# Performance work log

Hardware: AMD Instinct MI355X
Metric: run time of the kernel (lower is better)

Reference implementation:

```python
import jax, jax.numpy as jnp
import numpy as np
from jax import lax

N_SAMPLES = 2 ** 15   # 32768
N_ATOMS = 2048
ATOM_SIZE = 1024
K_SPARSE = 64
BATCH = 4


def setup_inputs() -> dict:
    key = jax.random.key(0)
    k1, k2 = jax.random.split(key)
    orig = jax.random.normal(k1, (BATCH, 1, N_SAMPLES), dtype=jnp.float32)
    # atoms ~ uniform(-1, 1) as in the torch Parameter init
    atoms = jax.random.uniform(k2, (N_ATOMS, ATOM_SIZE), dtype=jnp.float32,
                               minval=-1.0, maxval=1.0)
    return {"orig": orig, "atoms": atoms}


def reference(orig, atoms):
    B = orig.shape[0]
    # Correlate input with the atom dictionary (F.conv1d, padding=atom_size//2).
    x = lax.conv_general_dilated(
        orig, atoms.reshape(N_ATOMS, 1, ATOM_SIZE),
        window_strides=(1,), padding=[(ATOM_SIZE // 2, ATOM_SIZE // 2)],
        dimension_numbers=("NCH", "OIH", "NCH"))  # [B, n_atoms, N+1]
    x = x[..., :N_SAMPLES]                          # [B, n_atoms, N]
    # dropout(p=0.05) omitted (eval-mode / deterministic reference)

    # sparsify: per-batch top-k over the flattened (atom, time) grid
    flat = x.reshape(B, N_ATOMS * N_SAMPLES)
    values, indices = lax.top_k(flat, K_SPARSE)      # [B, K]
    atom_idx = indices // N_SAMPLES                  # [B, K]
    time_idx = indices % N_SAMPLES                   # [B, K]

    # Overlap-add synthesis: gather atom, scale, scatter-add into 2N buffer.
    contrib = atoms[atom_idx] * values[..., None]    # [B, K, atom_size]
    pos = time_idx[..., None] + jnp.arange(ATOM_SIZE)  # [B, K, atom_size]
    b_idx = jnp.arange(B)[:, None, None]
    out = jnp.zeros((B, 2 * N_SAMPLES), dtype=orig.dtype)
    out = out.at[b_idx, pos].add(contrib)
    return out[:, None, :N_SAMPLES]                  # [B, 1, N]
```

## Files before the change

### kernel.cpp

```cpp
#include <hip/hip_runtime.h>

#define NS     32768
#define NA     2048
#define ASZ    1024
#define NB     4
#define SIGC   34848
#define BM     128
#define BN     256
#define TILES  2048
#define CAP    8192
#define MINT   5080
#define SSCALE 20.0f
#define BSTR   1408
#define BSZ    22528

typedef signed char s8;
typedef __attribute__((ext_vector_type(4))) int i32x4;

__device__ __forceinline__ int imax(int a, int b) { return a > b ? a : b; }

__global__ void prep_k(const float* __restrict__ atoms, const float* __restrict__ orig,
                       s8* __restrict__ apack, s8* __restrict__ sigsh,
                       float* __restrict__ sigf, int* __restrict__ wlc) {
  if (blockIdx.x == 0 && threadIdx.x == 0) *wlc = 0;
  if (blockIdx.x < 1024) {
    int g = blockIdx.x >> 3, kt = blockIdx.x & 7;
    int t = threadIdx.x;
    int kk = t >> 7, r = t & 127, l = r >> 1, half = r & 1;
    int row = g * 16 + (l & 15);
    int kbase = kt * 128 + (kk * 4 + (l >> 4)) * 16 + half * 8;
    const float* srow = atoms + (size_t)row * ASZ + kbase;
    s8* dst = apack + (size_t)(((g * 8 + kt) * 2 + kk) << 10) + l * 16 + half * 8;
    #pragma unroll
    for (int j = 0; j < 8; j++) {
      float q = fminf(127.f, fmaxf(-127.f, srow[j] * 127.f));
      dst[j] = (s8)__float2int_rn(q);
    }
  } else {
    int r = blockIdx.x - 1024;
    int nch = (SIGC + 255) / 256;
    int bm = r / nch, chunk = r % nch;
    int i = chunk * 256 + threadIdx.x;
    if (i >= SIGC) return;
    int b = bm >> 4, m = bm & 15;
    int j = i + m - 512;
    float f = (j >= 0 && j < NS) ? orig[(size_t)b * NS + j] : 0.0f;
    float q = fminf(127.f, fmaxf(-127.f, f * SSCALE));
    sigsh[(size_t)bm * SIGC + i] = (s8)__float2int_rn(q);
    if (m == 0) sigf[(size_t)b * SIGC + i] = f;
  }
}

__device__ __forceinline__ void stage_bsig(const s8* __restrict__ Sb, int t0,
                                           s8* Bsig, int w, int lane) {
  #pragma unroll
  for (int i = 0; i < 3; i++) {
    int c = w + 8 * i;
    if (c < 22) {
      int o = c * 1024 + lane * 16;
      int m = o / BSTR;
      int pp = (o - m * BSTR) >> 4;
      int s = (pp & ~7) | ((pp ^ m) & 7);
      const s8* src = Sb + (size_t)m * SIGC + t0 + (s << 4);
      __builtin_amdgcn_global_load_lds((const __attribute__((address_space(1))) void*)src,
          (__attribute__((address_space(3))) void*)(&Bsig[c * 1024]), 16, 0, 0);
    }
  }
}

__device__ __forceinline__ void compute_tile(const s8* __restrict__ Apk, const s8* Bsig, int kt,
                                             int w, int lane, i32x4 acc[4][4]) {
  int wr = w >> 2, wc = w & 3;
  int kgrp = lane >> 4;
  int m = lane & 15, mx = m & 7;
  const s8* brow = Bsig + m * BSTR;
  const s8* abase = Apk + ((((size_t)wr * 4 * 8 + kt) * 2) << 10) + (lane << 4);
  int sb = wc * 4 + kgrp + kt * 8;
  #pragma unroll
  for (int kk = 0; kk < 2; kk++) {
    i32x4 af[4], bfr[4];
    #pragma unroll
    for (int mf = 0; mf < 4; mf++)
      af[mf] = *(const i32x4*)&abase[((mf * 16 + kk) << 10)];
    #pragma unroll
    for (int nf = 0; nf < 4; nf++) {
      int s = sb + nf + kk * 4;
      int ps = (s & ~7) | ((s ^ mx) & 7);
      bfr[nf] = *(const i32x4*)&brow[ps << 4];
    }
    __builtin_amdgcn_s_setprio(1);
    #pragma unroll
    for (int mf = 0; mf < 4; mf++)
      #pragma unroll
      for (int nf = 0; nf < 4; nf++)
        acc[mf][nf] = __builtin_amdgcn_mfma_i32_16x16x64_i8(af[mf], bfr[nf], acc[mf][nf], 0, 0, 0);
    __builtin_amdgcn_s_setprio(0);
  }
}

__global__ __launch_bounds__(512, 4)
void screen1(const s8* __restrict__ apack, const s8* __restrict__ sigsh,
             int* __restrict__ tmax)
{
  __shared__ __align__(16) s8 Bsig[BSZ];
  __shared__ int wred[8];
  int bid0 = blockIdx.x;
  int bid  = (bid0 & 7) * ((NB * TILES) >> 3) + (bid0 >> 3);
  int b = bid >> 11, tile = bid & (TILES - 1);
  int mt = tile >> 7, nt = tile & 127;
  int m0 = mt * BM, t0 = nt * BN;
  int tid = threadIdx.x, w = tid >> 6, lane = tid & 63;
  const s8* Apk = apack + (size_t)mt * 131072;
  const s8* Sb = sigsh + (size_t)b * 16 * SIGC;

  i32x4 acc[4][4];
  #pragma unroll
  for (int i = 0; i < 4; i++)
    #pragma unroll
    for (int j = 0; j < 4; j++) acc[i][j] = (i32x4){0, 0, 0, 0};

  stage_bsig(Sb, t0, Bsig, w, lane);
  __syncthreads();
  #pragma unroll 2
  for (int kt = 0; kt < 8; kt++)
    compute_tile(Apk, Bsig, kt, w, lane, acc);

  int lmax = -2147483647;
  #pragma unroll
  for (int mf = 0; mf < 4; mf++)
    #pragma unroll
    for (int nf = 0; nf < 4; nf++)
      #pragma unroll
      for (int q = 0; q < 4; q++) lmax = imax(lmax, acc[mf][nf][q]);
  #pragma unroll
  for (int off = 32; off; off >>= 1) lmax = imax(lmax, __shfl_xor(lmax, off, 64));
  if (lane == 0) wred[w] = lmax;
  __syncthreads();
  if (tid == 0) {
    int mm = wred[0];
    #pragma unroll
    for (int i = 1; i < 8; i++) mm = imax(mm, wred[i]);
    tmax[b * TILES + tile] = mm;
  }
}

__global__ void thresh_k(const int* __restrict__ tmax, int* __restrict__ thr,
                         int* __restrict__ ccnt, int* __restrict__ wl, int* __restrict__ wlc) {
  int b = blockIdx.x, tid = threadIdx.x;
  __shared__ int hist[4096];
  __shared__ int tsum[256];
  __shared__ int hist2[256];
  __shared__ int sB1, sAbove, sThr;
  for (int i = tid; i < 4096; i += 256) hist[i] = 0;
  __syncthreads();
  for (int i = tid; i < TILES; i += 256) {
    unsigned u = (unsigned)tmax[b * TILES + i] ^ 0x80000000u;
    atomicAdd(&hist[u >> 20], 1);
  }
  __syncthreads();
  { int s = 0;
    for (int j = 0; j < 16; j++) s += hist[tid * 16 + j];
    tsum[tid] = s; }
  __syncthreads();
  if (tid == 0) {
    int cum = 0, T = 0;
    for (int t2 = 255; t2 >= 0; t2--) {
      if (cum + tsum[t2] >= 64) { T = t2; break; }
      cum += tsum[t2];
    }
    int B1 = T * 16;
    for (int bk = T * 16 + 15; bk >= T * 16; bk--) {
      if (cum + hist[bk] >= 64) { B1 = bk; break; }
      cum += hist[bk];
    }
    sB1 = B1; sAbove = cum;
  }
  __syncthreads();
  if (tid < 256) hist2[tid] = 0;
  __syncthreads();
  int B1 = sB1;
  for (int i = tid; i < TILES; i += 256) {
    unsigned u = (unsigned)tmax[b * TILES + i] ^ 0x80000000u;
    if ((int)(u >> 20) == B1) atomicAdd(&hist2[(u >> 12) & 255], 1);
  }
  __syncthreads();
  if (tid == 0) {
    int cum = sAbove, B2 = 0;
    for (int z = 255; z >= 0; z--) { cum += hist2[z]; if (cum >= 64) { B2 = z; break; } }
    unsigned ulow = ((unsigned)B1 << 20) | ((unsigned)B2 << 12);
    int t = (int)(ulow ^ 0x80000000u);
    sThr = t; thr[b] = t; ccnt[b] = 0;
  }
  __syncthreads();
  int cut = sThr - MINT;
  for (int i = tid; i < TILES; i += 256)
    if (tmax[b * TILES + i] >= cut) { int p = atomicAdd(wlc, 1); wl[p] = (b << 11) | i; }
}

__global__ __launch_bounds__(512, 4)
void screen2(const s8* __restrict__ apack, const s8* __restrict__ sigsh,
             const int* __restrict__ thr, const int* __restrict__ wl,
             const int* __restrict__ wlc, int* __restrict__ ccnt, int* __restrict__ cidx)
{
  __shared__ __align__(16) s8 Bsig[BSZ];
  int n = *wlc; if (n > NB * TILES) n = NB * TILES;
  int tid = threadIdx.x, w = tid >> 6, lane = tid & 63;
  int wr = w >> 2, wc = w & 3;
  int kgrp = lane >> 4;

  for (int wi = blockIdx.x; wi < n; wi += gridDim.x) {
    int e = wl[wi];
    int b = e >> 11, tile = e & (TILES - 1);
    int cut = thr[b] - MINT;
    int mt = tile >> 7, nt = tile & 127;
    int m0 = mt * BM, t0 = nt * BN;
    const s8* Apk = apack + (size_t)mt * 131072;
    const s8* Sb = sigsh + (size_t)b * 16 * SIGC;

    i32x4 acc[4][4];
    #pragma unroll
    for (int i = 0; i < 4; i++)
      #pragma unroll
      for (int j = 0; j < 4; j++) acc[i][j] = (i32x4){0, 0, 0, 0};

    stage_bsig(Sb, t0, Bsig, w, lane);
    __syncthreads();
    #pragma unroll 2
    for (int kt = 0; kt < 8; kt++)
      compute_tile(Apk, Bsig, kt, w, lane, acc);

    int rb = m0 + wr * 64 + 4 * kgrp;
    int cb = t0 + wc * 64 + (lane & 15);
    #pragma unroll
    for (int mf = 0; mf < 4; mf++)
      #pragma unroll
      for (int nf = 0; nf < 4; nf++)
        #pragma unroll
        for (int q = 0; q < 4; q++) {
          if (acc[mf][nf][q] >= cut) {
            int a = rb + mf * 16 + q;
            int t = cb + nf * 16;
            int p = atomicAdd(&ccnt[b], 1);
            if (p < CAP) cidx[b * CAP + p] = (a << 15) | t;
          }
        }
    __syncthreads();
  }
}

__global__ void rescore_k(const float* __restrict__ atoms, const float* __restrict__ sigf,
                          const int* __restrict__ ccnt, const int* __restrict__ cidx,
                          float* __restrict__ cval) {
  int nwv = gridDim.x * 4;
  int gw = blockIdx.x * 4 + (threadIdx.x >> 6);
  int lane = threadIdx.x & 63;
  for (int b = 0; b < NB; b++) {
    int cnt = ccnt[b]; if (cnt > CAP) cnt = CAP;
    for (int ci = gw; ci < cnt; ci += nwv) {
      int idx = cidx[b * CAP + ci];
      int a = idx >> 15, t = idx & (NS - 1);
      const float* ap = atoms + (size_t)a * ASZ;
      const float* sp = sigf + (size_t)b * SIGC + t;
      float sum = 0.f;
      #pragma unroll
      for (int j = 0; j < 16; j++) { int k = lane + 64 * j; sum += ap[k] * sp[k]; }
      #pragma unroll
      for (int off = 32; off; off >>= 1) sum += __shfl_xor(sum, off, 64);
      if (lane == 0) cval[b * CAP + ci] = sum;
    }
  }
}

__global__ void select_k(const int* __restrict__ ccnt, const float* __restrict__ cval,
                         const int* __restrict__ cidx, float* __restrict__ sval,
                         int* __restrict__ sidx) {
  int b = blockIdx.x, tid = threadIdx.x;
  int cnt = ccnt[b]; if (cnt > CAP) cnt = CAP;
  __shared__ float lv[2048];
  __shared__ int li[2048];
  for (int ii = 0; ii * 256 < cnt; ii++) {
    int i = ii * 256 + tid;
    float vi = 0.f; int idi = 0; bool act = i < cnt;
    if (act) { vi = cval[b * CAP + i]; idi = cidx[b * CAP + i]; }
    int rank = 0;
    for (int c0 = 0; c0 < cnt; c0 += 2048) {
      int mchunk = cnt - c0; if (mchunk > 2048) mchunk = 2048;
      __syncthreads();
      for (int j = tid; j < mchunk; j += 256) {
        lv[j] = cval[b * CAP + c0 + j];
        li[j] = cidx[b * CAP + c0 + j];
      }
      __syncthreads();
      if (act)
        for (int j = 0; j < mchunk; j++)
          rank += (lv[j] > vi) || (lv[j] == vi && li[j] < idi);
    }
    if (act && rank < 64) { sval[b * 64 + rank] = vi; sidx[b * 64 + rank] = idi; }
  }
}

__global__ void recon_k(const float* __restrict__ atoms, const float* __restrict__ sval,
                        const int* __restrict__ sidx, float* __restrict__ out) {
  int gp = blockIdx.x * 256 + threadIdx.x;
  int b = gp >> 15, p = gp & (NS - 1);
  __shared__ float vv[64];
  __shared__ int ii[64];
  if (threadIdx.x < 64) {
    vv[threadIdx.x] = sval[b * 64 + threadIdx.x];
    ii[threadIdx.x] = sidx[b * 64 + threadIdx.x];
  }
  __syncthreads();
  float acc = 0.f;
  for (int s = 0; s < 64; s++) {
    int idx = ii[s];
    int a = idx >> 15, t = idx & (NS - 1);
    int off = p - t;
    if (off >= 0 && off < ASZ) acc += vv[s] * atoms[(size_t)a * ASZ + off];
  }
  out[gp] = acc;
}

extern "C" void kernel_launch(void* const* d_in, const int* in_sizes, int n_in,
                              void* d_out, int out_size, void* d_ws, size_t ws_size,
                              hipStream_t stream) {
  const float* orig  = (const float*)d_in[0];
  const float* atoms = (const float*)d_in[1];
  float* out = (float*)d_out;
  char* ws = (char*)d_ws;

  s8*    apack = (s8*)   (ws + 0);
  s8*    sigsh = (s8*)   (ws + 2097152);
  float* sigf  = (float*)(ws + 4327424);
  int*   tmax  = (int*)  (ws + 4884992);
  int*   thr   = (int*)  (ws + 4917760);
  int*   ccnt  = (int*)  (ws + 4918016);
  float* cval  = (float*)(ws + 4918272);
  int*   cidx  = (int*)  (ws + 5049344);
  float* sval  = (float*)(ws + 5180416);
  int*   sidx  = (int*)  (ws + 5181440);
  int*   wl    = (int*)  (ws + 5182464);
  int*   wlc   = (int*)  (ws + 5215232);

  int nch = (SIGC + 255) / 256;
  prep_k<<<1024 + NB * 16 * nch, 256, 0, stream>>>(atoms, orig, apack, sigsh, sigf, wlc);
  screen1<<<NB * TILES, 512, 0, stream>>>(apack, sigsh, tmax);
  thresh_k<<<NB, 256, 0, stream>>>(tmax, thr, ccnt, wl, wlc);
  screen2<<<256, 512, 0, stream>>>(apack, sigsh, thr, wl, wlc, ccnt, cidx);
  rescore_k<<<128, 256, 0, stream>>>(atoms, sigf, ccnt, cidx, cval);
  select_k<<<NB, 256, 0, stream>>>(ccnt, cval, cidx, sval, sidx);
  recon_k<<<out_size / 256, 256, 0, stream>>>(atoms, sval, sidx, out);
}
```

Measured before the change: 269.7 us.

## Widen screening tiles and make screen1 persistent with double-buffered signal staging

Doubles the time-tile width to 512 samples and uses 1024-thread workgroups with 16 waves, so each A-fragment load feeds twice as many columns. screen1 becomes a persistent kernel of 256 workgroups that prefetches the next tile's shifted signal into a second LDS buffer while computing the current one. This aims to cut A-matrix reload traffic and hide LDS staging latency. In exchange it uses more LDS per block, lowers occupancy, adds an extra barrier per tile, and screen2 now processes coarser worklist tiles, which may include more wasted work past the threshold.

Measured after the change: 281.8 us. +4.5%, slower.

```diff
diff --git a/kernel.cpp b/kernel.cpp
--- a/kernel.cpp
+++ b/kernel.cpp
@@ -6,13 +6,14 @@
 #define NB     4
 #define SIGC   34848
 #define BM     128
-#define BN     256
-#define TILES  2048
+#define BN     512
+#define TILES  1024
+#define NWG    4096
 #define CAP    8192
 #define MINT   5080
 #define SSCALE 20.0f
-#define BSTR   1408
-#define BSZ    22528
+#define BSTR   1664
+#define BSZ    26624
 
 typedef signed char s8;
 typedef __attribute__((ext_vector_type(4))) int i32x4;
@@ -54,9 +55,9 @@
 __device__ __forceinline__ void stage_bsig(const s8* __restrict__ Sb, int t0,
                                            s8* Bsig, int w, int lane) {
   #pragma unroll
-  for (int i = 0; i < 3; i++) {
-    int c = w + 8 * i;
-    if (c < 22) {
+  for (int i = 0; i < 2; i++) {
+    int c = w + 16 * i;
+    if (c < 26) {
       int o = c * 1024 + lane * 16;
       int m = o / BSTR;
       int pp = (o - m * BSTR) >> 4;
@@ -70,7 +71,7 @@
 
 __device__ __forceinline__ void compute_tile(const s8* __restrict__ Apk, const s8* Bsig, int kt,
                                              int w, int lane, i32x4 acc[4][4]) {
-  int wr = w >> 2, wc = w & 3;
+  int wr = w >> 3, wc = w & 7;
   int kgrp = lane >> 4;
   int m = lane & 15, mx = m & 7;
   const s8* brow = Bsig + m * BSTR;
@@ -98,49 +99,60 @@
   }
 }
 
-__global__ __launch_bounds__(512, 4)
+#define DECODE(x, b_, mt_, nt_) { int bb = ((x) & 7) * (NWG >> 3) + ((x) >> 3); \
+  b_ = bb >> 10; int tl = bb & (TILES - 1); mt_ = tl >> 6; nt_ = tl & 63; }
+
+__global__ __launch_bounds__(1024, 4)
 void screen1(const s8* __restrict__ apack, const s8* __restrict__ sigsh,
              int* __restrict__ tmax)
 {
-  __shared__ __align__(16) s8 Bsig[BSZ];
-  __shared__ int wred[8];
-  int bid0 = blockIdx.x;
-  int bid  = (bid0 & 7) * ((NB * TILES) >> 3) + (bid0 >> 3);
-  int b = bid >> 11, tile = bid & (TILES - 1);
-  int mt = tile >> 7, nt = tile & 127;
-  int m0 = mt * BM, t0 = nt * BN;
+  __shared__ __align__(16) s8 Bsig[2][BSZ];
+  __shared__ int wred[16];
   int tid = threadIdx.x, w = tid >> 6, lane = tid & 63;
-  const s8* Apk = apack + (size_t)mt * 131072;
-  const s8* Sb = sigsh + (size_t)b * 16 * SIGC;
-
-  i32x4 acc[4][4];
-  #pragma unroll
-  for (int i = 0; i < 4; i++)
-    #pragma unroll
-    for (int j = 0; j < 4; j++) acc[i][j] = (i32x4){0, 0, 0, 0};
-
-  stage_bsig(Sb, t0, Bsig, w, lane);
-  __syncthreads();
-  #pragma unroll 2
-  for (int kt = 0; kt < 8; kt++)
-    compute_tile(Apk, Bsig, kt, w, lane, acc);
-
-  int lmax = -2147483647;
-  #pragma unroll
-  for (int mf = 0; mf < 4; mf++)
-    #pragma unroll
-    for (int nf = 0; nf < 4; nf++)
-      #pragma unroll
-      for (int q = 0; q < 4; q++) lmax = imax(lmax, acc[mf][nf][q]);
-  #pragma unroll
-  for (int off = 32; off; off >>= 1) lmax = imax(lmax, __shfl_xor(lmax, off, 64));
-  if (lane == 0) wred[w] = lmax;
-  __syncthreads();
-  if (tid == 0) {
-    int mm = wred[0];
-    #pragma unroll
-    for (int i = 1; i < 8; i++) mm = imax(mm, wred[i]);
-    tmax[b * TILES + tile] = mm;
+
+  int b, mt, nt;
+  DECODE(blockIdx.x, b, mt, nt);
+  stage_bsig(sigsh + (size_t)b * 16 * SIGC, nt * BN, Bsig[0], w, lane);
+  __syncthreads();
+  int cur = 0;
+
+  for (int x = blockIdx.x; x < NWG; x += 256) {
+    int xn = x + 256;
+    int bn = 0, mtn = 0, ntn = 0;
+    if (xn < NWG) {
+      DECODE(xn, bn, mtn, ntn);
+      stage_bsig(sigsh + (size_t)bn * 16 * SIGC, ntn * BN, Bsig[cur ^ 1], w, lane);
+    }
+
+    const s8* Apk = apack + (size_t)mt * 131072;
+    i32x4 acc[4][4];
+    #pragma unroll
+    for (int i = 0; i < 4; i++)
+      #pragma unroll
+      for (int j = 0; j < 4; j++) acc[i][j] = (i32x4){0, 0, 0, 0};
+    #pragma unroll 2
+    for (int kt = 0; kt < 8; kt++)
+      compute_tile(Apk, Bsig[cur], kt, w, lane, acc);
+
+    int lmax = -2147483647;
+    #pragma unroll
+    for (int mf = 0; mf < 4; mf++)
+      #pragma unroll
+      for (int nf = 0; nf < 4; nf++)
+        #pragma unroll
+        for (int q = 0; q < 4; q++) lmax = imax(lmax, acc[mf][nf][q]);
+    #pragma unroll
+    for (int off = 32; off; off >>= 1) lmax = imax(lmax, __shfl_xor(lmax, off, 64));
+    if (lane == 0) wred[w] = lmax;
+    __syncthreads();
+    if (tid == 0) {
+      int mm = wred[0];
+      #pragma unroll
+      for (int i = 1; i < 16; i++) mm = imax(mm, wred[i]);
+      tmax[b * TILES + (mt << 6 | nt)] = mm;
+    }
+    __syncthreads();
+    cur ^= 1; b = bn; mt = mtn; nt = ntn;
   }
 }
 
@@ -194,25 +206,25 @@
   __syncthreads();
   int cut = sThr - MINT;
   for (int i = tid; i < TILES; i += 256)
-    if (tmax[b * TILES + i] >= cut) { int p = atomicAdd(wlc, 1); wl[p] = (b << 11) | i; }
-}
-
-__global__ __launch_bounds__(512, 4)
+    if (tmax[b * TILES + i] >= cut) { int p = atomicAdd(wlc, 1); wl[p] = (b << 10) | i; }
+}
+
+__global__ __launch_bounds__(1024, 4)
 void screen2(const s8* __restrict__ apack, const s8* __restrict__ sigsh,
              const int* __restrict__ thr, const int* __restrict__ wl,
              const int* __restrict__ wlc, int* __restrict__ ccnt, int* __restrict__ cidx)
 {
   __shared__ __align__(16) s8 Bsig[BSZ];
-  int n = *wlc; if (n > NB * TILES) n = NB * TILES;
+  int n = *wlc; if (n > NWG) n = NWG;
   int tid = threadIdx.x, w = tid >> 6, lane = tid & 63;
-  int wr = w >> 2, wc = w & 3;
+  int wr = w >> 3, wc = w & 7;
   int kgrp = lane >> 4;
 
   for (int wi = blockIdx.x; wi < n; wi += gridDim.x) {
     int e = wl[wi];
-    int b = e >> 11, tile = e & (TILES - 1);
+    int b = e >> 10, tile = e & (TILES - 1);
     int cut = thr[b] - MINT;
-    int mt = tile >> 7, nt = tile & 127;
+    int mt = tile >> 6, nt = tile & 63;
     int m0 = mt * BM, t0 = nt * BN;
     const s8* Apk = apack + (size_t)mt * 131072;
     const s8* Sb = sigsh + (size_t)b * 16 * SIGC;
@@ -332,20 +344,20 @@
   s8*    sigsh = (s8*)   (ws + 2097152);
   float* sigf  = (float*)(ws + 4327424);
   int*   tmax  = (int*)  (ws + 4884992);
-  int*   thr   = (int*)  (ws + 4917760);
-  int*   ccnt  = (int*)  (ws + 4918016);
-  float* cval  = (float*)(ws + 4918272);
-  int*   cidx  = (int*)  (ws + 5049344);
-  float* sval  = (float*)(ws + 5180416);
-  int*   sidx  = (int*)  (ws + 5181440);
-  int*   wl    = (int*)  (ws + 5182464);
-  int*   wlc   = (int*)  (ws + 5215232);
+  int*   thr   = (int*)  (ws + 4901376);
+  int*   ccnt  = (int*)  (ws + 4901632);
+  float* cval  = (float*)(ws + 4901888);
+  int*   cidx  = (int*)  (ws + 5032960);
+  float* sval  = (float*)(ws + 5164032);
+  int*   sidx  = (int*)  (ws + 5165056);
+  int*   wl    = (int*)  (ws + 5166080);
+  int*   wlc   = (int*)  (ws + 5182464);
 
   int nch = (SIGC + 255) / 256;
   prep_k<<<1024 + NB * 16 * nch, 256, 0, stream>>>(atoms, orig, apack, sigsh, sigf, wlc);
-  screen1<<<NB * TILES, 512, 0, stream>>>(apack, sigsh, tmax);
+  screen1<<<256, 1024, 0, stream>>>(apack, sigsh, tmax);
   thresh_k<<<NB, 256, 0, stream>>>(tmax, thr, ccnt, wl, wlc);
-  screen2<<<256, 512, 0, stream>>>(apack, sigsh, thr, wl, wlc, ccnt, cidx);
+  screen2<<<256, 1024, 0, stream>>>(apack, sigsh, thr, wl, wlc, ccnt, cidx);
   rescore_k<<<128, 256, 0, stream>>>(atoms, sigf, ccnt, cidx, cval);
   select_k<<<NB, 256, 0, stream>>>(ccnt, cval, cidx, sval, sidx);
   recon_k<<<out_size / 256, 256, 0, stream>>>(atoms, sval, sidx, out);
```

## Make screen1 persistent with double-buffered signal staging across tiles

Applied to the files above, without the earlier changes.

Screen1 moves from one workgroup per tile (8192 blocks) to 512 persistent workgroups that loop over tiles. The next tile's signal window is staged into a second LDS buffer while the current tile's MFMA work runs, to overlap global loads with compute and cut launch and prologue cost. The cost is that LDS use doubles (about 45 KB per block), which may lower occupancy. An extra barrier per iteration and a fixed grid that may not evenly fill the CUs add further risk.

Result: slower. 278.7 us (+3.3%).

```diff
diff --git a/kernel.cpp b/kernel.cpp
--- a/kernel.cpp
+++ b/kernel.cpp
@@ -8,6 +8,7 @@
 #define BM     128
 #define BN     256
 #define TILES  2048
+#define NWG    8192
 #define CAP    8192
 #define MINT   5080
 #define SSCALE 20.0f
@@ -98,49 +99,60 @@
   }
 }
 
+#define DECODE(x, b_, mt_, nt_) { int bb = ((x) & 7) * (NWG >> 3) + ((x) >> 3); \
+  b_ = bb >> 11; int tl = bb & (TILES - 1); mt_ = tl >> 7; nt_ = tl & 127; }
+
 __global__ __launch_bounds__(512, 4)
 void screen1(const s8* __restrict__ apack, const s8* __restrict__ sigsh,
              int* __restrict__ tmax)
 {
-  __shared__ __align__(16) s8 Bsig[BSZ];
+  __shared__ __align__(16) s8 Bsig[2][BSZ];
   __shared__ int wred[8];
-  int bid0 = blockIdx.x;
-  int bid  = (bid0 & 7) * ((NB * TILES) >> 3) + (bid0 >> 3);
-  int b = bid >> 11, tile = bid & (TILES - 1);
-  int mt = tile >> 7, nt = tile & 127;
-  int m0 = mt * BM, t0 = nt * BN;
   int tid = threadIdx.x, w = tid >> 6, lane = tid & 63;
-  const s8* Apk = apack + (size_t)mt * 131072;
-  const s8* Sb = sigsh + (size_t)b * 16 * SIGC;
-
-  i32x4 acc[4][4];
-  #pragma unroll
-  for (int i = 0; i < 4; i++)
-    #pragma unroll
-    for (int j = 0; j < 4; j++) acc[i][j] = (i32x4){0, 0, 0, 0};
-
-  stage_bsig(Sb, t0, Bsig, w, lane);
-  __syncthreads();
-  #pragma unroll 2
-  for (int kt = 0; kt < 8; kt++)
-    compute_tile(Apk, Bsig, kt, w, lane, acc);
-
-  int lmax = -2147483647;
-  #pragma unroll
-  for (int mf = 0; mf < 4; mf++)
-    #pragma unroll
-    for (int nf = 0; nf < 4; nf++)
-      #pragma unroll
-      for (int q = 0; q < 4; q++) lmax = imax(lmax, acc[mf][nf][q]);
-  #pragma unroll
-  for (int off = 32; off; off >>= 1) lmax = imax(lmax, __shfl_xor(lmax, off, 64));
-  if (lane == 0) wred[w] = lmax;
-  __syncthreads();
-  if (tid == 0) {
-    int mm = wred[0];
-    #pragma unroll
-    for (int i = 1; i < 8; i++) mm = imax(mm, wred[i]);
-    tmax[b * TILES + tile] = mm;
+
+  int b, mt, nt;
+  DECODE(blockIdx.x, b, mt, nt);
+  stage_bsig(sigsh + (size_t)b * 16 * SIGC, nt * BN, Bsig[0], w, lane);
+  __syncthreads();
+  int cur = 0;
+
+  for (int x = blockIdx.x; x < NWG; x += 512) {
+    int xn = x + 512;
+    int bn = 0, mtn = 0, ntn = 0;
+    if (xn < NWG) {
+      DECODE(xn, bn, mtn, ntn);
+      stage_bsig(sigsh + (size_t)bn * 16 * SIGC, ntn * BN, Bsig[cur ^ 1], w, lane);
+    }
+
+    const s8* Apk = apack + (size_t)mt * 131072;
+    i32x4 acc[4][4];
+    #pragma unroll
+    for (int i = 0; i < 4; i++)
+      #pragma unroll
+      for (int j = 0; j < 4; j++) acc[i][j] = (i32x4){0, 0, 0, 0};
+    #pragma unroll 2
+    for (int kt = 0; kt < 8; kt++)
+      compute_tile(Apk, Bsig[cur], kt, w, lane, acc);
+
+    int lmax = -2147483647;
+    #pragma unroll
+    for (int mf = 0; mf < 4; mf++)
+      #pragma unroll
+      for (int nf = 0; nf < 4; nf++)
+        #pragma unroll
+        for (int q = 0; q < 4; q++) lmax = imax(lmax, acc[mf][nf][q]);
+    #pragma unroll
+    for (int off = 32; off; off >>= 1) lmax = imax(lmax, __shfl_xor(lmax, off, 64));
+    if (lane == 0) wred[w] = lmax;
+    __syncthreads();
+    if (tid == 0) {
+      int mm = wred[0];
+      #pragma unroll
+      for (int i = 1; i < 8; i++) mm = imax(mm, wred[i]);
+      tmax[b * TILES + (mt << 7 | nt)] = mm;
+    }
+    __syncthreads();
+    cur ^= 1; b = bn; mt = mtn; nt = ntn;
   }
 }
 
@@ -203,7 +215,7 @@
              const int* __restrict__ wlc, int* __restrict__ ccnt, int* __restrict__ cidx)
 {
   __shared__ __align__(16) s8 Bsig[BSZ];
-  int n = *wlc; if (n > NB * TILES) n = NB * TILES;
+  int n = *wlc; if (n > NWG) n = NWG;
   int tid = threadIdx.x, w = tid >> 6, lane = tid & 63;
   int wr = w >> 2, wc = w & 3;
   int kgrp = lane >> 4;
@@ -343,7 +355,7 @@
 
   int nch = (SIGC + 255) / 256;
   prep_k<<<1024 + NB * 16 * nch, 256, 0, stream>>>(atoms, orig, apack, sigsh, sigf, wlc);
-  screen1<<<NB * TILES, 512, 0, stream>>>(apack, sigsh, tmax);
+  screen1<<<512, 512, 0, stream>>>(apack, sigsh, tmax);
   thresh_k<<<NB, 256, 0, stream>>>(tmax, thr, ccnt, wl, wlc);
   screen2<<<256, 512, 0, stream>>>(apack, sigsh, thr, wl, wlc, ccnt, cidx);
   rescore_k<<<128, 256, 0, stream>>>(atoms, sigf, ccnt, cidx, cval);
```
